# Kernel optimization log

Measured on AMD Instinct MI355X. Metric: run time of the kernel, lower is better.

## Reference

```python
import jax, jax.numpy as jnp
import numpy as np

L = 5          # num_layer
D = 300        # emb_dim
N = 100000     # nodes
E = 250000     # edges
G = 4000       # graphs
EPS = 1e-5


def setup_inputs() -> dict:
    key = jax.random.key(0)
    ks = jax.random.split(key, 32)
    f = lambda k, shape, s=0.02: (jax.random.normal(k, shape, dtype=jnp.float32) * s)
    inp = {
        "x_atom": jax.random.randint(ks[0], (N,), 0, 120),
        "x_chir": jax.random.randint(ks[1], (N,), 0, 3),
        "src": jax.random.randint(ks[2], (E,), 0, N),
        "dst": jax.random.randint(ks[3], (E,), 0, N),
        "edge_type": jax.random.randint(ks[4], (E,), 0, 6),
        "edge_dir": jax.random.randint(ks[5], (E,), 0, 3),
        "batch": jnp.sort(jax.random.randint(ks[6], (N,), 0, G)),
        # node feature embeddings
        "x_emb1": f(ks[7], (120, D), 0.1),
        "x_emb2": f(ks[8], (3, D), 0.1),
        # per-layer GIN params (stacked over L)
        "edge_e1": f(ks[9], (L, 6, D), 0.1),
        "edge_e2": f(ks[10], (L, 3, D), 0.1),
        "mlp_w1": f(ks[11], (L, D, 2 * D)),
        "mlp_b1": jnp.zeros((L, 2 * D), jnp.float32),
        "mlp_w2": f(ks[12], (L, 2 * D, D)),
        "mlp_b2": jnp.zeros((L, D), jnp.float32),
        # BatchNorm (inference mode: running stats)
        "bn_gamma": jnp.ones((L, D), jnp.float32),
        "bn_beta": jnp.zeros((L, D), jnp.float32),
        "bn_mean": f(ks[13], (L, D), 0.1),
        "bn_var": jax.random.uniform(ks[14], (L, D), jnp.float32, 0.5, 1.5),
        # virtual node (embedding initialized to zero in the original)
        "vn_emb": jnp.zeros((D,), jnp.float32),
        # vn MLPs: Linear -> LayerNorm -> ReLU -> Linear, L-1 of them
        "vn_w1": f(ks[15], (L - 1, D, D)),
        "vn_b1": jnp.zeros((L - 1, D), jnp.float32),
        "vn_ln_g": jnp.ones((L - 1, D), jnp.float32),
        "vn_ln_b": jnp.zeros((L - 1, D), jnp.float32),
        "vn_w2": f(ks[16], (L - 1, D, D)),
        "vn_b2": jnp.zeros((L - 1, D), jnp.float32),
    }
    return inp


def _forward(x_atom, x_chir, src, dst, edge_type, edge_dir, batch,
             x_emb1, x_emb2, edge_e1, edge_e2, mlp_w1, mlp_b1, mlp_w2, mlp_b2,
             bn_gamma, bn_beta, bn_mean, bn_var,
             vn_emb, vn_w1, vn_b1, vn_ln_g, vn_ln_b, vn_w2, vn_b2):
    n = x_atom.shape[0]
    # node counts per graph for mean pooling (guard empty graphs)
    counts = jnp.maximum(
        jax.ops.segment_sum(jnp.ones((n, 1), jnp.float32), batch, num_segments=G), 1.0)

    h = x_emb1[x_atom] + x_emb2[x_chir]                      # [N, D]
    vn_h = jnp.broadcast_to(vn_emb, (G, D))                  # [G, D]
    h = h + vn_h[batch]

    for l in range(L):
        # --- GIN conv: message = h[src] + edge_emb, scatter-add to dst ---
        edge_emb = edge_e1[l][edge_type] + edge_e2[l][edge_dir]   # [E, D]
        msg = h[src] + edge_emb
        aggr = jax.ops.segment_sum(msg, dst, num_segments=n)      # [N, D]
        # self loops: x_j = h[i], self-loop attr = (type 4, dir 0)
        aggr = aggr + h + (edge_e1[l][4] + edge_e2[l][0])
        # MLP: Linear(D,2D) -> ReLU -> Linear(2D,D)
        z = jax.nn.relu(aggr @ mlp_w1[l] + mlp_b1[l]) @ mlp_w2[l] + mlp_b2[l]
        # BatchNorm1d (eval): running stats
        z = (z - bn_mean[l]) * (bn_gamma[l] * jax.lax.rsqrt(bn_var[l] + EPS)) + bn_beta[l]
        if l < L - 1:
            z = jax.nn.relu(z)  # (dropout is identity at inference)
            # --- virtual node update ---
            pooled = jax.ops.segment_sum(z, batch, num_segments=G) / counts
            vn_new = pooled + vn_h                                # [G, D]
            t = vn_new @ vn_w1[l] + vn_b1[l]
            mu = jnp.mean(t, axis=-1, keepdims=True)
            var = jnp.var(t, axis=-1, keepdims=True)
            t = (t - mu) * jax.lax.rsqrt(var + EPS) * vn_ln_g[l] + vn_ln_b[l]
            vn_h = jax.nn.relu(t) @ vn_w2[l] + vn_b2[l]
            z = z + vn_h[batch]
        h = z
    return h


def reference(x_atom, x_chir, src, dst, edge_type, edge_dir, batch,
              x_emb1, x_emb2, edge_e1, edge_e2, mlp_w1, mlp_b1, mlp_w2, mlp_b2,
              bn_gamma, bn_beta, bn_mean, bn_var,
              vn_emb, vn_w1, vn_b1, vn_ln_g, vn_ln_b, vn_w2, vn_b2):
    return _forward(x_atom, x_chir, src, dst, edge_type, edge_dir, batch,
                    x_emb1, x_emb2, edge_e1, edge_e2, mlp_w1, mlp_b1, mlp_w2, mlp_b2,
                    bn_gamma, bn_beta, bn_mean, bn_var,
                    vn_emb, vn_w1, vn_b1, vn_ln_g, vn_ln_b, vn_w2, vn_b2)
```

## Files before the change

kernel.cpp:

```cpp
#include <hip/hip_runtime.h>

#define DD   300
#define DD2  600
#define GG   4000
#define GPAD 4096
#define LL   5
#define BN_EPS 1e-5f

typedef float f32x4  __attribute__((ext_vector_type(4)));
typedef short bf16x8 __attribute__((ext_vector_type(8)));

__device__ __forceinline__ unsigned short f2bf(float f) {
    unsigned int x = __float_as_uint(f);
    unsigned int r = (x + 0x7FFFu + ((x >> 16) & 1u)) >> 16;
    return (unsigned short)r;
}

__global__ __launch_bounds__(256) void k_hist(const int* __restrict__ idx, int* __restrict__ cnt, int n) {
    int i = blockIdx.x * 256 + threadIdx.x;
    if (i < n) atomicAdd(&cnt[idx[i]], 1);
}

__global__ __launch_bounds__(256) void k_scan1(const int* __restrict__ in, int* __restrict__ bsum, int n) {
    int t = threadIdx.x;
    int i = blockIdx.x * 256 + t;
    int v = (i < n) ? in[i] : 0;
    for (int off = 32; off >= 1; off >>= 1) v += __shfl_down(v, off, 64);
    __shared__ int s[4];
    if ((t & 63) == 0) s[t >> 6] = v;
    __syncthreads();
    if (t == 0) bsum[blockIdx.x] = s[0] + s[1] + s[2] + s[3];
}
__global__ __launch_bounds__(1024) void k_scan2(int* __restrict__ bsum, int nb) {
    __shared__ int s[1024];
    int t = threadIdx.x;
    int v = (t < nb) ? bsum[t] : 0;
    s[t] = v;
    __syncthreads();
    for (int off = 1; off < 1024; off <<= 1) {
        int u = (t >= off) ? s[t - off] : 0;
        __syncthreads();
        s[t] += u;
        __syncthreads();
    }
    if (t < nb) bsum[t] = s[t] - v;
}
__global__ __launch_bounds__(256) void k_scan3(const int* __restrict__ in, const int* __restrict__ boff,
                                               int* __restrict__ out, int n, int total) {
    __shared__ int s[256];
    int t = threadIdx.x;
    int i = blockIdx.x * 256 + t;
    int v = (i < n) ? in[i] : 0;
    s[t] = v;
    __syncthreads();
    for (int off = 1; off < 256; off <<= 1) {
        int u = (t >= off) ? s[t - off] : 0;
        __syncthreads();
        s[t] += u;
        __syncthreads();
    }
    if (i < n) out[i] = boff[blockIdx.x] + s[t] - v;
    if (i == 0) out[n] = total;
}

__global__ __launch_bounds__(256) void k_place(const int* __restrict__ src, const int* __restrict__ dst,
                                               const int* __restrict__ ety, const int* __restrict__ edir,
                                               const int* __restrict__ rowptr, int* __restrict__ cursor,
                                               int* __restrict__ einfo, int E) {
    int e = blockIdx.x * 256 + threadIdx.x;
    if (e >= E) return;
    int d = dst[e];
    int pos = rowptr[d] + atomicAdd(&cursor[d], 1);
    einfo[pos] = src[e] | ((ety[e] * 3 + edir[e]) << 20);
}

__global__ __launch_bounds__(256) void k_comb(const float* __restrict__ e1, const float* __restrict__ e2,
                                              float* __restrict__ comb) {
    int c = blockIdx.x, l = blockIdx.y;
    const float* r1 = e1 + ((size_t)l * 6 + (c / 3)) * DD;
    const float* r2 = e2 + ((size_t)l * 3 + (c % 3)) * DD;
    float* out = comb + ((size_t)l * 18 + c) * DD;
    for (int d = threadIdx.x; d < DD; d += 256) out[d] = r1[d] + r2[d];
}

__global__ __launch_bounds__(256) void k_init_h(const int* __restrict__ xa, const int* __restrict__ xc,
                                                const float* __restrict__ emb1, const float* __restrict__ emb2,
                                                const float* __restrict__ vne,
                                                float* __restrict__ h, int N) {
    int n = blockIdx.x;
    if (n >= N) return;
    int a = xa[n], c = xc[n];
    for (int d = threadIdx.x; d < DD; d += 256)
        h[(size_t)n * DD + d] = emb1[(size_t)a * DD + d] + emb2[(size_t)c * DD + d] + vne[d];
}

__global__ __launch_bounds__(256) void k_init_vn(const float* __restrict__ vne, float* __restrict__ vnh) {
    int g = blockIdx.x;
    for (int d = threadIdx.x; d < DD; d += 256) vnh[(size_t)g * DD + d] = vne[d];
}

__global__ __launch_bounds__(256) void k_aggr(const float* __restrict__ h,
                                              const int* __restrict__ rowptr, const int* __restrict__ einfo,
                                              const float* __restrict__ comb,
                                              const int* __restrict__ batch, const float* __restrict__ vnh,
                                              int use_vn,
                                              unsigned short* __restrict__ aggrb, int N, int Npad) {
    const int node = blockIdx.x * 4 + (threadIdx.x >> 6);
    const int lane = threadIdx.x & 63;
    if (node >= Npad) return;
    unsigned short* out = aggrb + (size_t)node * 320;
    if (node >= N) {
#pragma unroll
        for (int j = 0; j < 5; j++) out[lane + 64 * j] = 0;
        return;
    }
    float acc[5];
    const float* sc = comb + 12 * DD;
    const int p0 = rowptr[node], p1 = rowptr[node + 1];
    if (use_vn) {
        {
            const float* hs = h + (size_t)node * DD;
            const float* vs = vnh + (size_t)batch[node] * DD;
#pragma unroll
            for (int j = 0; j < 5; j++) {
                int d = lane + 64 * j;
                acc[j] = (d < DD) ? hs[d] + sc[d] + vs[d] : 0.f;
            }
        }
        for (int p = p0; p < p1; p++) {
            int info = einfo[p];
            int s = info & 0xFFFFF;
            const float* hr = h + (size_t)s * DD;
            const float* cr = comb + (size_t)(info >> 20) * DD;
            const float* vr = vnh + (size_t)batch[s] * DD;
#pragma unroll
            for (int j = 0; j < 5; j++) {
                int d = lane + 64 * j;
                if (d < DD) acc[j] += hr[d] + cr[d] + vr[d];
            }
        }
    } else {
        {
            const float* hs = h + (size_t)node * DD;
#pragma unroll
            for (int j = 0; j < 5; j++) {
                int d = lane + 64 * j;
                acc[j] = (d < DD) ? hs[d] + sc[d] : 0.f;
            }
        }
        for (int p = p0; p < p1; p++) {
            int info = einfo[p];
            const float* hr = h + (size_t)(info & 0xFFFFF) * DD;
            const float* cr = comb + (size_t)(info >> 20) * DD;
#pragma unroll
            for (int j = 0; j < 5; j++) {
                int d = lane + 64 * j;
                if (d < DD) acc[j] += hr[d] + cr[d];
            }
        }
    }
#pragma unroll
    for (int j = 0; j < 5; j++) {
        int d = lane + 64 * j;
        out[d] = (d < DD) ? f2bf(acc[j]) : (unsigned short)0;
    }
}

__global__ __launch_bounds__(256) void k_convw(const float* __restrict__ w, short* __restrict__ wt,
                                               int K, int Nn, int KP, int NP) {
    int n = blockIdx.x;
    int l = blockIdx.y;
    const float* wl = w + (size_t)l * K * Nn;
    short* wtl = wt + (size_t)l * NP * KP;
    for (int k = threadIdx.x; k < KP; k += 256) {
        float v = (k < K && n < Nn) ? wl[(size_t)k * Nn + n] : 0.f;
        wtl[(size_t)n * KP + k] = (short)f2bf(v);
    }
}

__global__ __launch_bounds__(256) void k_padb(const float* __restrict__ b, float* __restrict__ bp) {
    int l = blockIdx.y;
    int n = blockIdx.x * 256 + threadIdx.x;
    if (n < 640) bp[(size_t)l * 640 + n] = (n < DD2) ? b[(size_t)l * DD2 + n] : 0.f;
}


#define LD3(PTR, STRIDE, ROWBASE, KOFF)                                                                     \
    do {                                                                                                    \
        v0 = *(const float4*)((PTR) + (size_t)((ROWBASE) + (t >> 2)) * (STRIDE) + (KOFF) + (t & 3) * 8);    \
        v1 = *(const float4*)((PTR) + (size_t)((ROWBASE) + (t >> 2) + 64) * (STRIDE) + (KOFF) + (t & 3) * 8); \
        if (t < 128)                                                                                        \
            v2 = *(const float4*)((PTR) + (size_t)((ROWBASE) + (t >> 2) + 128) * (STRIDE) + (KOFF) + (t & 3) * 8); \
    } while (0)

#define ST3(BUF)                                                    \
    do {                                                            \
        *(float4*)&sB[BUF][t >> 2][(t & 3) * 8] = v0;               \
        *(float4*)&sB[BUF][(t >> 2) + 64][(t & 3) * 8] = v1;        \
        if (t < 128) *(float4*)&sB[BUF][(t >> 2) + 128][(t & 3) * 8] = v2; \
    } while (0)

__global__ __launch_bounds__(256, 2) void k_mlp(const unsigned short* __restrict__ aggrb,
                                                const short* __restrict__ w1t,
                                                const float* __restrict__ b1p,
                                                const short* __restrict__ w2t,
                                                const float* __restrict__ b2,
                                                const float* __restrict__ bng, const float* __restrict__ bnb,
                                                const float* __restrict__ bnm, const float* __restrict__ bnv,
                                                float* __restrict__ h, int N, int relu_out) {
    __shared__ short sH[64][168];
    __shared__ short sB[2][160][40];

    const int t    = threadIdx.x;
    const int m0   = blockIdx.x * 64;
    const int lane = t & 63;
    const int wv   = t >> 6;
    const int mi   = wv >> 1;
    const int ni   = wv & 1;
    const int col  = lane & 15;
    const int kq   = lane >> 4;
    const int kb   = kq << 3;

    bf16x8 areg[2][10];
    {
        const unsigned short* ap = aggrb + (size_t)(m0 + mi * 32 + col) * 320 + kb;
#pragma unroll
        for (int ks = 0; ks < 10; ks++) {
            areg[0][ks] = *(const bf16x8*)(ap + ks * 32);
            areg[1][ks] = *(const bf16x8*)(ap + (size_t)16 * 320 + ks * 32);
        }
        float4 v0, v1, v2;
        LD3(w1t, 320, 0, 0);
        ST3(0);
    }
    __syncthreads();

    f32x4 zacc[2][10];
#pragma unroll
    for (int f = 0; f < 2; f++)
#pragma unroll
        for (int j = 0; j < 10; j++) zacc[f][j] = (f32x4){0.f, 0.f, 0.f, 0.f};

#pragma unroll 1
    for (int ch = 0; ch < 4; ch++) {
        f32x4 hacc[2][5];
#pragma unroll
        for (int f = 0; f < 2; f++)
#pragma unroll
            for (int j = 0; j < 5; j++) hacc[f][j] = (f32x4){0.f, 0.f, 0.f, 0.f};

#pragma unroll
        for (int ks = 0; ks < 10; ks++) {
            float4 v0, v1, v2;
            if (ks < 9) LD3(w1t, 320, ch * 160, (ks + 1) * 32);
            else        LD3(w2t, 640, 0, ch * 160);
#pragma unroll
            for (int nt = 0; nt < 5; nt++) {
                bf16x8 b = *(const bf16x8*)&sB[ks & 1][ni * 80 + (nt << 4) + col][kb];
                hacc[0][nt] = __builtin_amdgcn_mfma_f32_16x16x32_bf16(areg[0][ks], b, hacc[0][nt], 0, 0, 0);
                hacc[1][nt] = __builtin_amdgcn_mfma_f32_16x16x32_bf16(areg[1][ks], b, hacc[1][nt], 0, 0, 0);
            }
            ST3((ks & 1) ^ 1);
            if (ks == 9) {
#pragma unroll
                for (int nt = 0; nt < 5; nt++) {
                    int cc = ni * 80 + (nt << 4) + col;
                    float bias = b1p[ch * 160 + cc];
#pragma unroll
                    for (int f = 0; f < 2; f++) {
#pragma unroll
                        for (int r = 0; r < 4; r++)
                            sH[mi * 32 + f * 16 + (kq << 2) + r][cc] =
                                (short)f2bf(fmaxf(hacc[f][nt][r] + bias, 0.f));
                    }
                }
            }
            __syncthreads();
        }

#pragma unroll
        for (int s = 0; s < 10; s++) {
            const int ks2 = s >> 1;
            float4 v0, v1, v2;
            bool stage = true;
            if (s < 9)       LD3(w2t, 640, ((s + 1) & 1) * 160, ch * 160 + ((s + 1) >> 1) * 32);
            else if (ch < 3) LD3(w1t, 320, (ch + 1) * 160, 0);
            else stage = false;
            if ((s & 1) == ni) {
                bf16x8 ha0 = *(const bf16x8*)&sH[mi * 32 + col][ks2 * 32 + kb];
                bf16x8 ha1 = *(const bf16x8*)&sH[mi * 32 + 16 + col][ks2 * 32 + kb];
#pragma unroll
                for (int jt = 0; jt < 10; jt++) {
                    bf16x8 b = *(const bf16x8*)&sB[s & 1][(jt << 4) + col][kb];
                    zacc[0][jt] = __builtin_amdgcn_mfma_f32_16x16x32_bf16(ha0, b, zacc[0][jt], 0, 0, 0);
                    zacc[1][jt] = __builtin_amdgcn_mfma_f32_16x16x32_bf16(ha1, b, zacc[1][jt], 0, 0, 0);
                }
            }
            if (stage) ST3((s & 1) ^ 1);
            __syncthreads();
        }
    }

#pragma unroll
    for (int jt = 0; jt < 10; jt++) {
        int n = ni * 160 + (jt << 4) + col;
        if (n < DD) {
            float bz = b2[n];
            float sc = bng[n] * rsqrtf(bnv[n] + BN_EPS);
            float mB = bnm[n], bB = bnb[n];
#pragma unroll
            for (int f = 0; f < 2; f++) {
                int mbase = m0 + mi * 32 + f * 16 + (kq << 2);
#pragma unroll
                for (int r = 0; r < 4; r++) {
                    int m = mbase + r;
                    if (m < N) {
                        float z = (zacc[f][jt][r] + bz - mB) * sc + bB;
                        if (relu_out) z = fmaxf(z, 0.f);
                        h[(size_t)m * DD + n] = z;
                    }
                }
            }
        }
    }
}

__global__ __launch_bounds__(256) void k_pool2(const float* __restrict__ h, const int* __restrict__ gptr,
                                               const float* __restrict__ vnh,
                                               unsigned short* __restrict__ vnin) {
    int g = blockIdx.x, t = threadIdx.x;
    const int gs = gptr[g], ge = gptr[g + 1];
    const float inv = 1.0f / fmaxf((float)(ge - gs), 1.0f);
    const int j0 = t, j1 = t + 256;
    const bool g1 = (j1 < DD);
    float a0 = 0.f, a1 = 0.f;
    for (int n = gs; n < ge; n++) {
        a0 += h[(size_t)n * DD + j0];
        if (g1) a1 += h[(size_t)n * DD + j1];
    }
    vnin[(size_t)g * 320 + j0] = f2bf(a0 * inv + vnh[(size_t)g * DD + j0]);
    if (j1 < 320)
        vnin[(size_t)g * 320 + j1] = g1 ? f2bf(a1 * inv + vnh[(size_t)g * DD + j1]) : (unsigned short)0;
}

__global__ __launch_bounds__(256) void k_vng(const unsigned short* __restrict__ A,
                                             const short* __restrict__ Wt,
                                             const float* __restrict__ bias,
                                             float* __restrict__ outf,
                                             int M) {
    __shared__ short sA[2][64][40];
    __shared__ short sB[2][160][40];
    const int t  = threadIdx.x;
    const int m0 = blockIdx.x * 64;
    const int n0 = blockIdx.y * 160;
    const int ar = t >> 2, aq = (t & 3) << 3;

    {
        *(float4*)&sA[0][ar][aq] = *(const float4*)(A + (size_t)(m0 + ar) * 320 + aq);
#pragma unroll
        for (int i = 0; i < 3; i++) {
            int c = t + (i << 8);
            if (c < 640) {
                int br = c >> 2, bq = (c & 3) << 3;
                *(float4*)&sB[0][br][bq] = *(const float4*)(Wt + (size_t)(n0 + br) * 320 + bq);
            }
        }
    }
    __syncthreads();

    const int lane = t & 63;
    const int w    = t >> 6;
    const int mrow = (w << 4) + (lane & 15);
    const int kb   = (lane >> 4) << 3;
    const int col  = lane & 15;
    const int rq   = (lane >> 4) << 2;

    f32x4 acc[10];
#pragma unroll
    for (int nt = 0; nt < 10; nt++) acc[nt] = (f32x4){0.f, 0.f, 0.f, 0.f};

    for (int ks = 0; ks < 10; ks++) {
        const int nb = ks & 1;
        const bool have = (ks + 1) < 10;
        float4 avr, bv0, bv1, bv2;
        if (have) {
            const int k0 = (ks + 1) << 5;
            avr = *(const float4*)(A + (size_t)(m0 + ar) * 320 + k0 + aq);
            int c = t;
            bv0 = *(const float4*)(Wt + (size_t)(n0 + (c >> 2)) * 320 + k0 + ((c & 3) << 3));
            c = t + 256;
            bv1 = *(const float4*)(Wt + (size_t)(n0 + (c >> 2)) * 320 + k0 + ((c & 3) << 3));
            if (t < 128) {
                c = t + 512;
                bv2 = *(const float4*)(Wt + (size_t)(n0 + (c >> 2)) * 320 + k0 + ((c & 3) << 3));
            }
        }
        bf16x8 a = *(const bf16x8*)&sA[nb][mrow][kb];
#pragma unroll
        for (int nt = 0; nt < 10; nt++) {
            bf16x8 b = *(const bf16x8*)&sB[nb][(nt << 4) + col][kb];
            acc[nt] = __builtin_amdgcn_mfma_f32_16x16x32_bf16(a, b, acc[nt], 0, 0, 0);
        }
        if (have) {
            *(float4*)&sA[nb ^ 1][ar][aq] = avr;
            int c = t;
            *(float4*)&sB[nb ^ 1][c >> 2][(c & 3) << 3] = bv0;
            c = t + 256;
            *(float4*)&sB[nb ^ 1][c >> 2][(c & 3) << 3] = bv1;
            if (t < 128) {
                c = t + 512;
                *(float4*)&sB[nb ^ 1][c >> 2][(c & 3) << 3] = bv2;
            }
        }
        __syncthreads();
    }

#pragma unroll
    for (int nt = 0; nt < 10; nt++) {
        int n = n0 + (nt << 4) + col;
        bool nok = (n < DD);
        float bz = nok ? bias[n] : 0.f;
        int mbase = m0 + (w << 4) + rq;
#pragma unroll
        for (int r = 0; r < 4; r++) {
            int m = mbase + r;
            if (nok && m < M)
                outf[(size_t)m * DD + n] = acc[nt][r] + bz;
        }
    }
}

__global__ __launch_bounds__(256) void k_ln(const float* __restrict__ tbuf,
                                            const float* __restrict__ lng, const float* __restrict__ lnb,
                                            unsigned short* __restrict__ vnrelu) {
    __shared__ float rs[4], rq[4];
    __shared__ float s_mu, s_rstd;
    int g = blockIdx.x, t = threadIdx.x;
    const int j0 = t, j1 = t + 256;
    const bool g1 = (j1 < DD);
    float t0 = tbuf[(size_t)g * DD + j0];
    float t1 = g1 ? tbuf[(size_t)g * DD + j1] : 0.f;
    float ps = t0 + t1;
    float pq = t0 * t0 + t1 * t1;
    for (int off = 32; off >= 1; off >>= 1) { ps += __shfl_down(ps, off, 64); pq += __shfl_down(pq, off, 64); }
    int wid = t >> 6, lane = t & 63;
    if (lane == 0) { rs[wid] = ps; rq[wid] = pq; }
    __syncthreads();
    if (t == 0) {
        float S = rs[0] + rs[1] + rs[2] + rs[3];
        float Q = rq[0] + rq[1] + rq[2] + rq[3];
        float mu = S / DD;
        float var = Q / DD - mu * mu;
        s_mu = mu;
        s_rstd = rsqrtf(var + BN_EPS);
    }
    __syncthreads();
    float mu = s_mu, rstd = s_rstd;
    float r0 = fmaxf((t0 - mu) * rstd * lng[j0] + lnb[j0], 0.f);
    vnrelu[(size_t)g * 320 + j0] = f2bf(r0);
    if (j1 < 320) {
        float r1 = g1 ? fmaxf((t1 - mu) * rstd * lng[j1] + lnb[j1], 0.f) : 0.f;
        vnrelu[(size_t)g * 320 + j1] = g1 ? f2bf(r1) : (unsigned short)0;
    }
}

extern "C" void kernel_launch(void* const* d_in, const int* in_sizes, int n_in,
                              void* d_out, int out_size, void* d_ws, size_t ws_size,
                              hipStream_t stream) {
    const int*   x_atom = (const int*)d_in[0];
    const int*   x_chir = (const int*)d_in[1];
    const int*   src    = (const int*)d_in[2];
    const int*   dst    = (const int*)d_in[3];
    const int*   ety    = (const int*)d_in[4];
    const int*   edir   = (const int*)d_in[5];
    const int*   batch  = (const int*)d_in[6];
    const float* emb1   = (const float*)d_in[7];
    const float* emb2   = (const float*)d_in[8];
    const float* e1     = (const float*)d_in[9];
    const float* e2     = (const float*)d_in[10];
    const float* w1     = (const float*)d_in[11];
    const float* b1     = (const float*)d_in[12];
    const float* w2     = (const float*)d_in[13];
    const float* b2     = (const float*)d_in[14];
    const float* bng    = (const float*)d_in[15];
    const float* bnb    = (const float*)d_in[16];
    const float* bnm    = (const float*)d_in[17];
    const float* bnv    = (const float*)d_in[18];
    const float* vne    = (const float*)d_in[19];
    const float* vw1    = (const float*)d_in[20];
    const float* vb1    = (const float*)d_in[21];
    const float* lng    = (const float*)d_in[22];
    const float* lnb    = (const float*)d_in[23];
    const float* vw2    = (const float*)d_in[24];
    const float* vb2    = (const float*)d_in[25];

    const int N = in_sizes[0];
    const int E = in_sizes[2];
    const int gx = (N + 63) / 64;
    const int Npad = gx * 64;
    const int nbN = (N + 255) / 256;
    const int nbG = (GG + 255) / 256;

    float* h = (float*)d_out;

    unsigned short* aggrb  = (unsigned short*)d_ws;
    unsigned short* hidden = aggrb + (size_t)Npad * 320;
    short*          w1t    = (short*)(hidden + (size_t)Npad * 640);
    short*          w2t    = w1t + (size_t)LL * 640 * 320;
    short*          vw1t   = w2t + (size_t)LL * 320 * 640;
    short*          vw2t   = vw1t + (size_t)(LL - 1) * 320 * 320;
    unsigned short* vnin   = (unsigned short*)(vw2t + (size_t)(LL - 1) * 320 * 320);
    unsigned short* vnrelu = vnin + (size_t)GPAD * 320;
    float*          b1p    = (float*)(vnrelu + (size_t)GPAD * 320);
    float*          comb   = b1p + (size_t)LL * 640;
    float*          tbuf   = comb + (size_t)LL * 18 * DD;
    float*          vnh    = tbuf + (size_t)GG * DD;
    int*            deg    = (int*)(vnh + (size_t)GG * DD);
    int*            cursor = deg + N;
    int*            gcnt   = cursor + N;
    int*            rowptr = gcnt + GG;
    int*            gptr   = rowptr + (N + 1);
    int*            bsumN  = gptr + (GG + 1);
    int*            bsumG  = bsumN + 1024;
    int*            einfo  = bsumG + 1024;

    k_convw<<<dim3(640, LL), 256, 0, stream>>>(w1, w1t, DD, DD2, 320, 640);
    k_convw<<<dim3(320, LL), 256, 0, stream>>>(w2, w2t, DD2, DD, 640, 320);
    k_convw<<<dim3(320, LL - 1), 256, 0, stream>>>(vw1, vw1t, DD, DD, 320, 320);
    k_convw<<<dim3(320, LL - 1), 256, 0, stream>>>(vw2, vw2t, DD, DD, 320, 320);
    k_padb<<<dim3(3, LL), 256, 0, stream>>>(b1, b1p);
    k_comb<<<dim3(18, LL), 256, 0, stream>>>(e1, e2, comb);

    hipMemsetAsync(deg, 0, (size_t)(2 * N + GG) * sizeof(int), stream);
    k_hist<<<(E + 255) / 256, 256, 0, stream>>>(dst, deg, E);
    k_hist<<<(N + 255) / 256, 256, 0, stream>>>(batch, gcnt, N);
    k_scan1<<<nbN, 256, 0, stream>>>(deg, bsumN, N);
    k_scan2<<<1, 1024, 0, stream>>>(bsumN, nbN);
    k_scan3<<<nbN, 256, 0, stream>>>(deg, bsumN, rowptr, N, E);
    k_scan1<<<nbG, 256, 0, stream>>>(gcnt, bsumG, GG);
    k_scan2<<<1, 1024, 0, stream>>>(bsumG, nbG);
    k_scan3<<<nbG, 256, 0, stream>>>(gcnt, bsumG, gptr, GG, N);
    k_place<<<(E + 255) / 256, 256, 0, stream>>>(src, dst, ety, edir, rowptr, cursor, einfo, E);

    k_init_h<<<N, 256, 0, stream>>>(x_atom, x_chir, emb1, emb2, vne, h, N);
    k_init_vn<<<GG, 256, 0, stream>>>(vne, vnh);

    for (int l = 0; l < LL; l++) {
        k_aggr<<<Npad / 4, 256, 0, stream>>>(h, rowptr, einfo, comb + (size_t)l * 18 * DD,
                                             batch, vnh, (l > 0) ? 1 : 0, aggrb, N, Npad);
        k_mlp<<<gx, 256, 0, stream>>>(aggrb, w1t + (size_t)l * 640 * 320,
                                      b1p + (size_t)l * 640,
                                      w2t + (size_t)l * 320 * 640,
                                      b2 + (size_t)l * DD,
                                      bng + (size_t)l * DD, bnb + (size_t)l * DD,
                                      bnm + (size_t)l * DD, bnv + (size_t)l * DD,
                                      h, N, (l < LL - 1) ? 1 : 0);
        if (l < LL - 1) {
            k_pool2<<<GG, 256, 0, stream>>>(h, gptr, vnh, vnin);
            k_vng<<<dim3(GPAD / 64, 2), 256, 0, stream>>>(vnin, vw1t + (size_t)l * 320 * 320,
                                                          vb1 + (size_t)l * DD, tbuf, GG);
            k_ln<<<GG, 256, 0, stream>>>(tbuf, lng + (size_t)l * DD, lnb + (size_t)l * DD, vnrelu);
            k_vng<<<dim3(GPAD / 64, 2), 256, 0, stream>>>(vnrelu, vw2t + (size_t)l * 320 * 320,
                                                          vb2 + (size_t)l * DD, vnh, GG);
        }
    }
}
```

Measured before the change: 2.150 ms.

## Stream MLP weight slices into LDS via direct global-to-LDS loads with triple buffering

The MLP weights are now pre-packed into contiguous 160x32 bf16 slices with an XOR swizzle, and the fused MLP kernel loads them straight into a 3-deep LDS ring using global_load_lds. This replaces the register-staged double buffer and __syncthreads with explicit waitcnt plus barrier. The aim is to prefetch two phases ahead, remove the VGPR round trip and store instructions, and avoid LDS bank conflicts through the swizzle. The risks are fragile hand-written vmcnt accounting and more LDS per block, which could reduce occupancy.

```diff
diff --git a/kernel.cpp b/kernel.cpp
--- a/kernel.cpp
+++ b/kernel.cpp
@@ -14,6 +14,12 @@
     unsigned int x = __float_as_uint(f);
     unsigned int r = (x + 0x7FFFu + ((x >> 16) & 1u)) >> 16;
     return (unsigned short)r;
+}
+
+__device__ __forceinline__ void gload16(const short* g, short* l) {
+    __builtin_amdgcn_global_load_lds(
+        (const __attribute__((address_space(1))) unsigned int*)(const void*)g,
+        (__attribute__((address_space(3))) unsigned int*)(void*)l, 16, 0, 0);
 }
 
 __global__ __launch_bounds__(256) void k_hist(const int* __restrict__ idx, int* __restrict__ cnt, int n) {
@@ -185,31 +191,65 @@
 }
 
 
-#define LD3(PTR, STRIDE, ROWBASE, KOFF)                                                                     \
-    do {                                                                                                    \
-        v0 = *(const float4*)((PTR) + (size_t)((ROWBASE) + (t >> 2)) * (STRIDE) + (KOFF) + (t & 3) * 8);    \
-        v1 = *(const float4*)((PTR) + (size_t)((ROWBASE) + (t >> 2) + 64) * (STRIDE) + (KOFF) + (t & 3) * 8); \
-        if (t < 128)                                                                                        \
-            v2 = *(const float4*)((PTR) + (size_t)((ROWBASE) + (t >> 2) + 128) * (STRIDE) + (KOFF) + (t & 3) * 8); \
+__global__ __launch_bounds__(256) void k_pack1(const float* __restrict__ w, short* __restrict__ out) {
+    const int sl = blockIdx.x, l = blockIdx.y;
+    const int ch = sl / 10, ks = sl % 10;
+    const float* wl = w + (size_t)l * DD * DD2;
+    short* ol = out + ((size_t)l * 40 + sl) * 5120;
+    for (int it = threadIdx.x; it < 640; it += 256) {
+        const int r = it >> 2, pq = it & 3;
+        const int q = pq ^ ((r >> 1) & 3);
+        const int nh = ch * 160 + r;
+        short* o = ol + (size_t)it * 8;
+#pragma unroll
+        for (int e = 0; e < 8; e++) {
+            const int k = ks * 32 + q * 8 + e;
+            float f = (k < DD && nh < DD2) ? wl[(size_t)k * DD2 + nh] : 0.f;
+            o[e] = (short)f2bf(f);
+        }
+    }
+}
+
+__global__ __launch_bounds__(256) void k_pack2(const float* __restrict__ w, short* __restrict__ out) {
+    const int sl = blockIdx.x, l = blockIdx.y;
+    const int ch = sl / 10, s = sl % 10;
+    const int half = s & 1, ks2 = s >> 1;
+    const float* wl = w + (size_t)l * DD2 * DD;
+    short* ol = out + ((size_t)l * 40 + sl) * 5120;
+    for (int it = threadIdx.x; it < 640; it += 256) {
+        const int r = it >> 2, pq = it & 3;
+        const int q = pq ^ ((r >> 1) & 3);
+        const int nout = half * 160 + r;
+        short* o = ol + (size_t)it * 8;
+#pragma unroll
+        for (int e = 0; e < 8; e++) {
+            const int khid = ch * 160 + ks2 * 32 + q * 8 + e;
+            float f = (khid < DD2 && nout < DD) ? wl[(size_t)khid * DD + nout] : 0.f;
+            o[e] = (short)f2bf(f);
+        }
+    }
+}
+
+
+#define ENDPHASE()                                                      \
+    do {                                                                \
+        asm volatile("s_waitcnt lgkmcnt(0)" ::: "memory");              \
+        if (wv < 2) asm volatile("s_waitcnt vmcnt(3)" ::: "memory");    \
+        else        asm volatile("s_waitcnt vmcnt(2)" ::: "memory");    \
+        __builtin_amdgcn_s_barrier();                                   \
+        asm volatile("" ::: "memory");                                  \
     } while (0)
 
-#define ST3(BUF)                                                    \
-    do {                                                            \
-        *(float4*)&sB[BUF][t >> 2][(t & 3) * 8] = v0;               \
-        *(float4*)&sB[BUF][(t >> 2) + 64][(t & 3) * 8] = v1;        \
-        if (t < 128) *(float4*)&sB[BUF][(t >> 2) + 128][(t & 3) * 8] = v2; \
-    } while (0)
-
 __global__ __launch_bounds__(256, 2) void k_mlp(const unsigned short* __restrict__ aggrb,
-                                                const short* __restrict__ w1t,
+                                                const short* __restrict__ w1s,
                                                 const float* __restrict__ b1p,
-                                                const short* __restrict__ w2t,
+                                                const short* __restrict__ w2s,
                                                 const float* __restrict__ b2,
                                                 const float* __restrict__ bng, const float* __restrict__ bnb,
                                                 const float* __restrict__ bnm, const float* __restrict__ bnv,
                                                 float* __restrict__ h, int N, int relu_out) {
+    __shared__ short sRing[3][160][32];
     __shared__ short sH[64][168];
-    __shared__ short sB[2][160][40];
 
     const int t    = threadIdx.x;
     const int m0   = blockIdx.x * 64;
@@ -220,6 +260,20 @@
     const int col  = lane & 15;
     const int kq   = lane >> 4;
     const int kb   = kq << 3;
+    const int pq8  = (kq ^ ((col >> 1) & 3)) << 3;
+
+    auto STAGE = [&](const short* src, int rg) {
+        short* dst = &sRing[rg][0][0];
+        gload16(src + (size_t)wv * 512 + lane * 8, dst + wv * 512 + lane * 8);
+        gload16(src + (size_t)(wv + 4) * 512 + lane * 8, dst + (wv + 4) * 512 + lane * 8);
+        if (wv < 2)
+            gload16(src + (size_t)(wv + 8) * 512 + lane * 8, dst + (wv + 8) * 512 + lane * 8);
+    };
+    auto SRC = [&](int pn) -> const short* {
+        int chn = pn / 20, in = pn % 20;
+        return (in < 10) ? (w1s + (size_t)(chn * 10 + in) * 5120)
+                         : (w2s + (size_t)(chn * 10 + (in - 10)) * 5120);
+    };
 
     bf16x8 areg[2][10];
     {
@@ -229,11 +283,12 @@
             areg[0][ks] = *(const bf16x8*)(ap + ks * 32);
             areg[1][ks] = *(const bf16x8*)(ap + (size_t)16 * 320 + ks * 32);
         }
-        float4 v0, v1, v2;
-        LD3(w1t, 320, 0, 0);
-        ST3(0);
-    }
-    __syncthreads();
+        STAGE(SRC(0), 0);
+        STAGE(SRC(1), 1);
+    }
+    asm volatile("s_waitcnt vmcnt(0) lgkmcnt(0)" ::: "memory");
+    __builtin_amdgcn_s_barrier();
+    asm volatile("" ::: "memory");
 
     f32x4 zacc[2][10];
 #pragma unroll
@@ -241,6 +296,7 @@
 #pragma unroll
         for (int j = 0; j < 10; j++) zacc[f][j] = (f32x4){0.f, 0.f, 0.f, 0.f};
 
+    int p = 0;
 #pragma unroll 1
     for (int ch = 0; ch < 4; ch++) {
         f32x4 hacc[2][5];
@@ -251,16 +307,16 @@
 
 #pragma unroll
         for (int ks = 0; ks < 10; ks++) {
-            float4 v0, v1, v2;
-            if (ks < 9) LD3(w1t, 320, ch * 160, (ks + 1) * 32);
-            else        LD3(w2t, 640, 0, ch * 160);
+            const int pn = p + 2;
+            if (pn < 80) STAGE(SRC(pn), pn % 3);
+            const int rg = p % 3;
+            const short* bb = &sRing[rg][ni * 80 + col][0] + pq8;
 #pragma unroll
             for (int nt = 0; nt < 5; nt++) {
-                bf16x8 b = *(const bf16x8*)&sB[ks & 1][ni * 80 + (nt << 4) + col][kb];
+                bf16x8 b = *(const bf16x8*)(bb + nt * 512);
                 hacc[0][nt] = __builtin_amdgcn_mfma_f32_16x16x32_bf16(areg[0][ks], b, hacc[0][nt], 0, 0, 0);
                 hacc[1][nt] = __builtin_amdgcn_mfma_f32_16x16x32_bf16(areg[1][ks], b, hacc[1][nt], 0, 0, 0);
             }
-            ST3((ks & 1) ^ 1);
             if (ks == 9) {
 #pragma unroll
                 for (int nt = 0; nt < 5; nt++) {
@@ -275,29 +331,29 @@
                     }
                 }
             }
-            __syncthreads();
+            ENDPHASE();
+            p++;
         }
 
 #pragma unroll
         for (int s = 0; s < 10; s++) {
-            const int ks2 = s >> 1;
-            float4 v0, v1, v2;
-            bool stage = true;
-            if (s < 9)       LD3(w2t, 640, ((s + 1) & 1) * 160, ch * 160 + ((s + 1) >> 1) * 32);
-            else if (ch < 3) LD3(w1t, 320, (ch + 1) * 160, 0);
-            else stage = false;
+            const int pn = p + 2;
+            if (pn < 80) STAGE(SRC(pn), pn % 3);
+            const int rg = p % 3;
             if ((s & 1) == ni) {
+                const int ks2 = s >> 1;
                 bf16x8 ha0 = *(const bf16x8*)&sH[mi * 32 + col][ks2 * 32 + kb];
                 bf16x8 ha1 = *(const bf16x8*)&sH[mi * 32 + 16 + col][ks2 * 32 + kb];
+                const short* bb = &sRing[rg][col][0] + pq8;
 #pragma unroll
                 for (int jt = 0; jt < 10; jt++) {
-                    bf16x8 b = *(const bf16x8*)&sB[s & 1][(jt << 4) + col][kb];
+                    bf16x8 b = *(const bf16x8*)(bb + jt * 512);
                     zacc[0][jt] = __builtin_amdgcn_mfma_f32_16x16x32_bf16(ha0, b, zacc[0][jt], 0, 0, 0);
                     zacc[1][jt] = __builtin_amdgcn_mfma_f32_16x16x32_bf16(ha1, b, zacc[1][jt], 0, 0, 0);
                 }
             }
-            if (stage) ST3((s & 1) ^ 1);
-            __syncthreads();
+            ENDPHASE();
+            p++;
         }
     }
 
@@ -505,9 +561,9 @@
 
     unsigned short* aggrb  = (unsigned short*)d_ws;
     unsigned short* hidden = aggrb + (size_t)Npad * 320;
-    short*          w1t    = (short*)(hidden + (size_t)Npad * 640);
-    short*          w2t    = w1t + (size_t)LL * 640 * 320;
-    short*          vw1t   = w2t + (size_t)LL * 320 * 640;
+    short*          w1s    = (short*)(hidden + (size_t)Npad * 640);
+    short*          w2s    = w1s + (size_t)LL * 640 * 320;
+    short*          vw1t   = w2s + (size_t)LL * 320 * 640;
     short*          vw2t   = vw1t + (size_t)(LL - 1) * 320 * 320;
     unsigned short* vnin   = (unsigned short*)(vw2t + (size_t)(LL - 1) * 320 * 320);
     unsigned short* vnrelu = vnin + (size_t)GPAD * 320;
@@ -524,8 +580,8 @@
     int*            bsumG  = bsumN + 1024;
     int*            einfo  = bsumG + 1024;
 
-    k_convw<<<dim3(640, LL), 256, 0, stream>>>(w1, w1t, DD, DD2, 320, 640);
-    k_convw<<<dim3(320, LL), 256, 0, stream>>>(w2, w2t, DD2, DD, 640, 320);
+    k_pack1<<<dim3(40, LL), 256, 0, stream>>>(w1, w1s);
+    k_pack2<<<dim3(40, LL), 256, 0, stream>>>(w2, w2s);
     k_convw<<<dim3(320, LL - 1), 256, 0, stream>>>(vw1, vw1t, DD, DD, 320, 320);
     k_convw<<<dim3(320, LL - 1), 256, 0, stream>>>(vw2, vw2t, DD, DD, 320, 320);
     k_padb<<<dim3(3, LL), 256, 0, stream>>>(b1, b1p);
@@ -548,9 +604,9 @@
     for (int l = 0; l < LL; l++) {
         k_aggr<<<Npad / 4, 256, 0, stream>>>(h, rowptr, einfo, comb + (size_t)l * 18 * DD,
                                              batch, vnh, (l > 0) ? 1 : 0, aggrb, N, Npad);
-        k_mlp<<<gx, 256, 0, stream>>>(aggrb, w1t + (size_t)l * 640 * 320,
+        k_mlp<<<gx, 256, 0, stream>>>(aggrb, w1s + (size_t)l * 40 * 5120,
                                       b1p + (size_t)l * 640,
-                                      w2t + (size_t)l * 320 * 640,
+                                      w2s + (size_t)l * 40 * 5120,
                                       b2 + (size_t)l * DD,
                                       bng + (size_t)l * DD, bnb + (size_t)l * DD,
                                       bnm + (size_t)l * DD, bnv + (size_t)l * DD,
```

Result: slower. 2.362 ms (+9.9%).

## Double MLP row tile to 128 with 512 threads and XOR-swizzled LDS

Applied to the files above, without the earlier changes.

The fused MLP kernel now handles 128 rows per block with 8 waves instead of 64 rows with 4. Each weight tile staged in shared memory is therefore reused across twice as many rows, and each thread loads fewer weight vectors. The padded shared-memory strides are replaced by an XOR swizzle on the column groups of sB and sH to avoid bank conflicts without padding. This halves the block count and raises per-block register and LDS pressure under launch_bounds(512,2), which risks lower occupancy or spills.

```diff
diff --git a/kernel.cpp b/kernel.cpp
--- a/kernel.cpp
+++ b/kernel.cpp
@@ -185,22 +185,24 @@
 }
 
 
-#define LD3(PTR, STRIDE, ROWBASE, KOFF)                                                                     \
+#define LD2(PTR, STRIDE, ROWBASE, KOFF)                                                                     \
     do {                                                                                                    \
         v0 = *(const float4*)((PTR) + (size_t)((ROWBASE) + (t >> 2)) * (STRIDE) + (KOFF) + (t & 3) * 8);    \
-        v1 = *(const float4*)((PTR) + (size_t)((ROWBASE) + (t >> 2) + 64) * (STRIDE) + (KOFF) + (t & 3) * 8); \
         if (t < 128)                                                                                        \
-            v2 = *(const float4*)((PTR) + (size_t)((ROWBASE) + (t >> 2) + 128) * (STRIDE) + (KOFF) + (t & 3) * 8); \
+            v1 = *(const float4*)((PTR) + (size_t)((ROWBASE) + (t >> 2) + 128) * (STRIDE) + (KOFF) + (t & 3) * 8); \
     } while (0)
 
-#define ST3(BUF)                                                    \
-    do {                                                            \
-        *(float4*)&sB[BUF][t >> 2][(t & 3) * 8] = v0;               \
-        *(float4*)&sB[BUF][(t >> 2) + 64][(t & 3) * 8] = v1;        \
-        if (t < 128) *(float4*)&sB[BUF][(t >> 2) + 128][(t & 3) * 8] = v2; \
+#define ST2(BUF)                                                                     \
+    do {                                                                             \
+        int r0_ = t >> 2, p0_ = (t & 3) ^ ((r0_ >> 1) & 3);                          \
+        *(float4*)&sB[BUF][r0_][p0_ * 8] = v0;                                       \
+        if (t < 128) {                                                               \
+            int r1_ = r0_ + 128, p1_ = (t & 3) ^ ((r1_ >> 1) & 3);                   \
+            *(float4*)&sB[BUF][r1_][p1_ * 8] = v1;                                   \
+        }                                                                            \
     } while (0)
 
-__global__ __launch_bounds__(256, 2) void k_mlp(const unsigned short* __restrict__ aggrb,
+__global__ __launch_bounds__(512, 2) void k_mlp(const unsigned short* __restrict__ aggrb,
                                                 const short* __restrict__ w1t,
                                                 const float* __restrict__ b1p,
                                                 const short* __restrict__ w2t,
@@ -208,11 +210,11 @@
                                                 const float* __restrict__ bng, const float* __restrict__ bnb,
                                                 const float* __restrict__ bnm, const float* __restrict__ bnv,
                                                 float* __restrict__ h, int N, int relu_out) {
-    __shared__ short sH[64][168];
-    __shared__ short sB[2][160][40];
+    __shared__ short sH[128][160];
+    __shared__ short sB[2][160][32];
 
     const int t    = threadIdx.x;
-    const int m0   = blockIdx.x * 64;
+    const int m0   = blockIdx.x * 128;
     const int lane = t & 63;
     const int wv   = t >> 6;
     const int mi   = wv >> 1;
@@ -220,6 +222,7 @@
     const int col  = lane & 15;
     const int kq   = lane >> 4;
     const int kb   = kq << 3;
+    const int bq   = (kq ^ ((col >> 1) & 3)) << 3;
 
     bf16x8 areg[2][10];
     {
@@ -229,9 +232,9 @@
             areg[0][ks] = *(const bf16x8*)(ap + ks * 32);
             areg[1][ks] = *(const bf16x8*)(ap + (size_t)16 * 320 + ks * 32);
         }
-        float4 v0, v1, v2;
-        LD3(w1t, 320, 0, 0);
-        ST3(0);
+        float4 v0, v1;
+        LD2(w1t, 320, 0, 0);
+        ST2(0);
     }
     __syncthreads();
 
@@ -251,27 +254,31 @@
 
 #pragma unroll
         for (int ks = 0; ks < 10; ks++) {
-            float4 v0, v1, v2;
-            if (ks < 9) LD3(w1t, 320, ch * 160, (ks + 1) * 32);
-            else        LD3(w2t, 640, 0, ch * 160);
+            float4 v0, v1;
+            if (ks < 9) LD2(w1t, 320, ch * 160, (ks + 1) * 32);
+            else        LD2(w2t, 640, 0, ch * 160);
 #pragma unroll
             for (int nt = 0; nt < 5; nt++) {
-                bf16x8 b = *(const bf16x8*)&sB[ks & 1][ni * 80 + (nt << 4) + col][kb];
+                bf16x8 b = *(const bf16x8*)&sB[ks & 1][ni * 80 + (nt << 4) + col][bq];
                 hacc[0][nt] = __builtin_amdgcn_mfma_f32_16x16x32_bf16(areg[0][ks], b, hacc[0][nt], 0, 0, 0);
                 hacc[1][nt] = __builtin_amdgcn_mfma_f32_16x16x32_bf16(areg[1][ks], b, hacc[1][nt], 0, 0, 0);
             }
-            ST3((ks & 1) ^ 1);
+            ST2((ks & 1) ^ 1);
             if (ks == 9) {
 #pragma unroll
                 for (int nt = 0; nt < 5; nt++) {
                     int cc = ni * 80 + (nt << 4) + col;
+                    int cchi = cc >> 3, cclo = cc & 7;
                     float bias = b1p[ch * 160 + cc];
 #pragma unroll
                     for (int f = 0; f < 2; f++) {
 #pragma unroll
-                        for (int r = 0; r < 4; r++)
-                            sH[mi * 32 + f * 16 + (kq << 2) + r][cc] =
+                        for (int r = 0; r < 4; r++) {
+                            int row = mi * 32 + f * 16 + (kq << 2) + r;
+                            int sw = ((kq << 1) + (r >> 1)) & 3;
+                            sH[row][((cchi ^ sw) << 3) + cclo] =
                                 (short)f2bf(fmaxf(hacc[f][nt][r] + bias, 0.f));
+                        }
                     }
                 }
             }
@@ -280,23 +287,23 @@
 
 #pragma unroll
         for (int s = 0; s < 10; s++) {
-            const int ks2 = s >> 1;
-            float4 v0, v1, v2;
+            float4 v0, v1;
             bool stage = true;
-            if (s < 9)       LD3(w2t, 640, ((s + 1) & 1) * 160, ch * 160 + ((s + 1) >> 1) * 32);
-            else if (ch < 3) LD3(w1t, 320, (ch + 1) * 160, 0);
+            if (s < 9)       LD2(w2t, 640, ((s + 1) & 1) * 160, ch * 160 + ((s + 1) >> 1) * 32);
+            else if (ch < 3) LD2(w1t, 320, (ch + 1) * 160, 0);
             else stage = false;
             if ((s & 1) == ni) {
-                bf16x8 ha0 = *(const bf16x8*)&sH[mi * 32 + col][ks2 * 32 + kb];
-                bf16x8 ha1 = *(const bf16x8*)&sH[mi * 32 + 16 + col][ks2 * 32 + kb];
+                const int ks2 = s >> 1;
+                bf16x8 ha0 = *(const bf16x8*)&sH[mi * 32 + col][ks2 * 32 + bq];
+                bf16x8 ha1 = *(const bf16x8*)&sH[mi * 32 + 16 + col][ks2 * 32 + bq];
 #pragma unroll
                 for (int jt = 0; jt < 10; jt++) {
-                    bf16x8 b = *(const bf16x8*)&sB[s & 1][(jt << 4) + col][kb];
+                    bf16x8 b = *(const bf16x8*)&sB[s & 1][(jt << 4) + col][bq];
                     zacc[0][jt] = __builtin_amdgcn_mfma_f32_16x16x32_bf16(ha0, b, zacc[0][jt], 0, 0, 0);
                     zacc[1][jt] = __builtin_amdgcn_mfma_f32_16x16x32_bf16(ha1, b, zacc[1][jt], 0, 0, 0);
                 }
             }
-            if (stage) ST3((s & 1) ^ 1);
+            if (stage) ST2((s & 1) ^ 1);
             __syncthreads();
         }
     }
@@ -496,8 +503,8 @@
 
     const int N = in_sizes[0];
     const int E = in_sizes[2];
-    const int gx = (N + 63) / 64;
-    const int Npad = gx * 64;
+    const int gx2 = (N + 127) / 128;
+    const int Npad = gx2 * 128;
     const int nbN = (N + 255) / 256;
     const int nbG = (GG + 255) / 256;
 
@@ -548,13 +555,13 @@
     for (int l = 0; l < LL; l++) {
         k_aggr<<<Npad / 4, 256, 0, stream>>>(h, rowptr, einfo, comb + (size_t)l * 18 * DD,
                                              batch, vnh, (l > 0) ? 1 : 0, aggrb, N, Npad);
-        k_mlp<<<gx, 256, 0, stream>>>(aggrb, w1t + (size_t)l * 640 * 320,
-                                      b1p + (size_t)l * 640,
-                                      w2t + (size_t)l * 320 * 640,
-                                      b2 + (size_t)l * DD,
-                                      bng + (size_t)l * DD, bnb + (size_t)l * DD,
-                                      bnm + (size_t)l * DD, bnv + (size_t)l * DD,
-                                      h, N, (l < LL - 1) ? 1 : 0);
+        k_mlp<<<gx2, 512, 0, stream>>>(aggrb, w1t + (size_t)l * 640 * 320,
+                                       b1p + (size_t)l * 640,
+                                       w2t + (size_t)l * 320 * 640,
+                                       b2 + (size_t)l * DD,
+                                       bng + (size_t)l * DD, bnb + (size_t)l * DD,
+                                       bnm + (size_t)l * DD, bnv + (size_t)l * DD,
+                                       h, N, (l < LL - 1) ? 1 : 0);
         if (l < LL - 1) {
             k_pool2<<<GG, 256, 0, stream>>>(h, gptr, vnh, vnin);
             k_vng<<<dim3(GPAD / 64, 2), 256, 0, stream>>>(vnin, vw1t + (size_t)l * 320 * 320,
```

After: 2.252 ms. +4.7%, slower.

## Store intermediate node features as bf16 and vectorize aggregation gather

Applied to the files above, without the earlier changes.

Intermediate node embeddings between layers are now stored as bf16 in a padded 320-wide buffer instead of fp32. The gather-heavy aggregation and the pooling kernels read half the bytes, and aggregation now loads packed pairs with 32-bit and float2 accesses. Only the last layer writes fp32 output. The trade-off is extra rounding of hidden states, an added memset of the bf16 buffer, and possible accuracy drift across layers.

```diff
diff --git a/kernel.cpp b/kernel.cpp
--- a/kernel.cpp
+++ b/kernel.cpp
@@ -14,6 +14,9 @@
     unsigned int x = __float_as_uint(f);
     unsigned int r = (x + 0x7FFFu + ((x >> 16) & 1u)) >> 16;
     return (unsigned short)r;
+}
+__device__ __forceinline__ float bf2f(unsigned short u) {
+    return __uint_as_float(((unsigned int)u) << 16);
 }
 
 __global__ __launch_bounds__(256) void k_hist(const int* __restrict__ idx, int* __restrict__ cnt, int n) {
@@ -86,12 +89,12 @@
 __global__ __launch_bounds__(256) void k_init_h(const int* __restrict__ xa, const int* __restrict__ xc,
                                                 const float* __restrict__ emb1, const float* __restrict__ emb2,
                                                 const float* __restrict__ vne,
-                                                float* __restrict__ h, int N) {
+                                                unsigned short* __restrict__ hbf, int N) {
     int n = blockIdx.x;
     if (n >= N) return;
     int a = xa[n], c = xc[n];
     for (int d = threadIdx.x; d < DD; d += 256)
-        h[(size_t)n * DD + d] = emb1[(size_t)a * DD + d] + emb2[(size_t)c * DD + d] + vne[d];
+        hbf[(size_t)n * 320 + d] = f2bf(emb1[(size_t)a * DD + d] + emb2[(size_t)c * DD + d] + vne[d]);
 }
 
 __global__ __launch_bounds__(256) void k_init_vn(const float* __restrict__ vne, float* __restrict__ vnh) {
@@ -99,7 +102,7 @@
     for (int d = threadIdx.x; d < DD; d += 256) vnh[(size_t)g * DD + d] = vne[d];
 }
 
-__global__ __launch_bounds__(256) void k_aggr(const float* __restrict__ h,
+__global__ __launch_bounds__(256) void k_aggr(const unsigned short* __restrict__ hbf,
                                               const int* __restrict__ rowptr, const int* __restrict__ einfo,
                                               const float* __restrict__ comb,
                                               const int* __restrict__ batch, const float* __restrict__ vnh,
@@ -108,62 +111,67 @@
     const int node = blockIdx.x * 4 + (threadIdx.x >> 6);
     const int lane = threadIdx.x & 63;
     if (node >= Npad) return;
-    unsigned short* out = aggrb + (size_t)node * 320;
+    unsigned int* out = (unsigned int*)(aggrb + (size_t)node * 320);
     if (node >= N) {
-#pragma unroll
-        for (int j = 0; j < 5; j++) out[lane + 64 * j] = 0;
+        out[lane] = 0u; out[lane + 64] = 0u;
+        if (lane < 32) out[lane + 128] = 0u;
         return;
     }
-    float acc[5];
-    const float* sc = comb + 12 * DD;
+    float aL0 = 0.f, aH0 = 0.f, aL1 = 0.f, aH1 = 0.f, aL2 = 0.f, aH2 = 0.f;
+    const int dp  = 2 * lane;
+    const bool l2a = (lane < 32);
+    const bool l2c = (lane < 22);
+
+#define ADDH(ROW)                                                              \
+    do {                                                                       \
+        const unsigned int* r_ = (const unsigned int*)(ROW);                   \
+        unsigned int v0_ = r_[lane], v1_ = r_[lane + 64];                      \
+        aL0 += __uint_as_float(v0_ << 16); aH0 += __uint_as_float(v0_ & 0xFFFF0000u); \
+        aL1 += __uint_as_float(v1_ << 16); aH1 += __uint_as_float(v1_ & 0xFFFF0000u); \
+        if (l2a) {                                                             \
+            unsigned int v2_ = r_[lane + 128];                                 \
+            aL2 += __uint_as_float(v2_ << 16); aH2 += __uint_as_float(v2_ & 0xFFFF0000u); \
+        }                                                                      \
+    } while (0)
+
+#define ADDF(ROW)                                                              \
+    do {                                                                       \
+        const float* r_ = (ROW);                                               \
+        float2 v0_ = *(const float2*)(r_ + dp);                                \
+        float2 v1_ = *(const float2*)(r_ + dp + 128);                          \
+        aL0 += v0_.x; aH0 += v0_.y;                                            \
+        aL1 += v1_.x; aH1 += v1_.y;                                            \
+        if (l2c) {                                                             \
+            float2 v2_ = *(const float2*)(r_ + dp + 256);                      \
+            aL2 += v2_.x; aH2 += v2_.y;                                        \
+        }                                                                      \
+    } while (0)
+
     const int p0 = rowptr[node], p1 = rowptr[node + 1];
+    ADDH(hbf + (size_t)node * 320);
+    ADDF(comb + 12 * DD);
     if (use_vn) {
-        {
-            const float* hs = h + (size_t)node * DD;
-            const float* vs = vnh + (size_t)batch[node] * DD;
-#pragma unroll
-            for (int j = 0; j < 5; j++) {
-                int d = lane + 64 * j;
-                acc[j] = (d < DD) ? hs[d] + sc[d] + vs[d] : 0.f;
-            }
-        }
+        ADDF(vnh + (size_t)batch[node] * DD);
         for (int p = p0; p < p1; p++) {
             int info = einfo[p];
             int s = info & 0xFFFFF;
-            const float* hr = h + (size_t)s * DD;
-            const float* cr = comb + (size_t)(info >> 20) * DD;
-            const float* vr = vnh + (size_t)batch[s] * DD;
-#pragma unroll
-            for (int j = 0; j < 5; j++) {
-                int d = lane + 64 * j;
-                if (d < DD) acc[j] += hr[d] + cr[d] + vr[d];
-            }
+            ADDH(hbf + (size_t)s * 320);
+            ADDF(comb + (size_t)(info >> 20) * DD);
+            ADDF(vnh + (size_t)batch[s] * DD);
         }
     } else {
-        {
-            const float* hs = h + (size_t)node * DD;
-#pragma unroll
-            for (int j = 0; j < 5; j++) {
-                int d = lane + 64 * j;
-                acc[j] = (d < DD) ? hs[d] + sc[d] : 0.f;
-            }
-        }
         for (int p = p0; p < p1; p++) {
             int info = einfo[p];
-            const float* hr = h + (size_t)(info & 0xFFFFF) * DD;
-            const float* cr = comb + (size_t)(info >> 20) * DD;
-#pragma unroll
-            for (int j = 0; j < 5; j++) {
-                int d = lane + 64 * j;
-                if (d < DD) acc[j] += hr[d] + cr[d];
-            }
-        }
-    }
-#pragma unroll
-    for (int j = 0; j < 5; j++) {
-        int d = lane + 64 * j;
-        out[d] = (d < DD) ? f2bf(acc[j]) : (unsigned short)0;
-    }
+            ADDH(hbf + (size_t)(info & 0xFFFFF) * 320);
+            ADDF(comb + (size_t)(info >> 20) * DD);
+        }
+    }
+#undef ADDH
+#undef ADDF
+    out[lane]      = ((unsigned int)f2bf(aH0) << 16) | f2bf(aL0);
+    out[lane + 64] = ((unsigned int)f2bf(aH1) << 16) | f2bf(aL1);
+    if (l2a)
+        out[lane + 128] = ((unsigned int)f2bf(aH2) << 16) | f2bf(aL2);
 }
 
 __global__ __launch_bounds__(256) void k_convw(const float* __restrict__ w, short* __restrict__ wt,
@@ -184,7 +192,6 @@
     if (n < 640) bp[(size_t)l * 640 + n] = (n < DD2) ? b[(size_t)l * DD2 + n] : 0.f;
 }
 
-
 #define LD3(PTR, STRIDE, ROWBASE, KOFF)                                                                     \
     do {                                                                                                    \
         v0 = *(const float4*)((PTR) + (size_t)((ROWBASE) + (t >> 2)) * (STRIDE) + (KOFF) + (t & 3) * 8);    \
@@ -207,7 +214,9 @@
                                                 const float* __restrict__ b2,
                                                 const float* __restrict__ bng, const float* __restrict__ bnb,
                                                 const float* __restrict__ bnm, const float* __restrict__ bnv,
-                                                float* __restrict__ h, int N, int relu_out) {
+                                                unsigned short* __restrict__ hbf,
+                                                float* __restrict__ hfin,
+                                                int N, int relu_out) {
     __shared__ short sH[64][168];
     __shared__ short sB[2][160][40];
 
@@ -316,8 +325,10 @@
                     int m = mbase + r;
                     if (m < N) {
                         float z = (zacc[f][jt][r] + bz - mB) * sc + bB;
-                        if (relu_out) z = fmaxf(z, 0.f);
-                        h[(size_t)m * DD + n] = z;
+                        if (relu_out)
+                            hbf[(size_t)m * 320 + n] = f2bf(fmaxf(z, 0.f));
+                        else
+                            hfin[(size_t)m * DD + n] = z;
                     }
                 }
             }
@@ -325,7 +336,8 @@
     }
 }
 
-__global__ __launch_bounds__(256) void k_pool2(const float* __restrict__ h, const int* __restrict__ gptr,
+__global__ __launch_bounds__(256) void k_pool2(const unsigned short* __restrict__ hbf,
+                                               const int* __restrict__ gptr,
                                                const float* __restrict__ vnh,
                                                unsigned short* __restrict__ vnin) {
     int g = blockIdx.x, t = threadIdx.x;
@@ -335,8 +347,8 @@
     const bool g1 = (j1 < DD);
     float a0 = 0.f, a1 = 0.f;
     for (int n = gs; n < ge; n++) {
-        a0 += h[(size_t)n * DD + j0];
-        if (g1) a1 += h[(size_t)n * DD + j1];
+        a0 += bf2f(hbf[(size_t)n * 320 + j0]);
+        if (g1) a1 += bf2f(hbf[(size_t)n * 320 + j1]);
     }
     vnin[(size_t)g * 320 + j0] = f2bf(a0 * inv + vnh[(size_t)g * DD + j0]);
     if (j1 < 320)
@@ -504,8 +516,8 @@
     float* h = (float*)d_out;
 
     unsigned short* aggrb  = (unsigned short*)d_ws;
-    unsigned short* hidden = aggrb + (size_t)Npad * 320;
-    short*          w1t    = (short*)(hidden + (size_t)Npad * 640);
+    unsigned short* hbf    = aggrb + (size_t)Npad * 320;
+    short*          w1t    = (short*)(hbf + (size_t)Npad * 640);
     short*          w2t    = w1t + (size_t)LL * 640 * 320;
     short*          vw1t   = w2t + (size_t)LL * 320 * 640;
     short*          vw2t   = vw1t + (size_t)(LL - 1) * 320 * 320;
@@ -532,6 +544,7 @@
     k_comb<<<dim3(18, LL), 256, 0, stream>>>(e1, e2, comb);
 
     hipMemsetAsync(deg, 0, (size_t)(2 * N + GG) * sizeof(int), stream);
+    hipMemsetAsync(hbf, 0, (size_t)Npad * 320 * sizeof(unsigned short), stream);
     k_hist<<<(E + 255) / 256, 256, 0, stream>>>(dst, deg, E);
     k_hist<<<(N + 255) / 256, 256, 0, stream>>>(batch, gcnt, N);
     k_scan1<<<nbN, 256, 0, stream>>>(deg, bsumN, N);
@@ -542,11 +555,11 @@
     k_scan3<<<nbG, 256, 0, stream>>>(gcnt, bsumG, gptr, GG, N);
     k_place<<<(E + 255) / 256, 256, 0, stream>>>(src, dst, ety, edir, rowptr, cursor, einfo, E);
 
-    k_init_h<<<N, 256, 0, stream>>>(x_atom, x_chir, emb1, emb2, vne, h, N);
+    k_init_h<<<N, 256, 0, stream>>>(x_atom, x_chir, emb1, emb2, vne, hbf, N);
     k_init_vn<<<GG, 256, 0, stream>>>(vne, vnh);
 
     for (int l = 0; l < LL; l++) {
-        k_aggr<<<Npad / 4, 256, 0, stream>>>(h, rowptr, einfo, comb + (size_t)l * 18 * DD,
+        k_aggr<<<Npad / 4, 256, 0, stream>>>(hbf, rowptr, einfo, comb + (size_t)l * 18 * DD,
                                              batch, vnh, (l > 0) ? 1 : 0, aggrb, N, Npad);
         k_mlp<<<gx, 256, 0, stream>>>(aggrb, w1t + (size_t)l * 640 * 320,
                                       b1p + (size_t)l * 640,
@@ -554,9 +567,9 @@
                                       b2 + (size_t)l * DD,
                                       bng + (size_t)l * DD, bnb + (size_t)l * DD,
                                       bnm + (size_t)l * DD, bnv + (size_t)l * DD,
-                                      h, N, (l < LL - 1) ? 1 : 0);
+                                      hbf, h, N, (l < LL - 1) ? 1 : 0);
         if (l < LL - 1) {
-            k_pool2<<<GG, 256, 0, stream>>>(h, gptr, vnh, vnin);
+            k_pool2<<<GG, 256, 0, stream>>>(hbf, gptr, vnh, vnin);
             k_vng<<<dim3(GPAD / 64, 2), 256, 0, stream>>>(vnin, vw1t + (size_t)l * 320 * 320,
                                                           vb1 + (size_t)l * DD, tbuf, GG);
             k_ln<<<GG, 256, 0, stream>>>(tbuf, lng + (size_t)l * DD, lnb + (size_t)l * DD, vnrelu);
```

Result: slower. 2.335 ms (+8.6%).
